# Optimization experiments

Measured on AMD Instinct MI355X. Metric: run time of the kernel, lower is better.

## Reference

```python
import jax, jax.numpy as jnp
import numpy as np

B, C, L, H, T, W = 512, 256, 256, 512, 16, 8  # batch, num_channels, seq_len, hidden_dim, timestep, windows


def setup_inputs() -> dict:
    key = jax.random.key(0)
    ks = jax.random.split(key, 8)
    s = 0.02
    return {
        "features_aug2": jax.random.normal(ks[0], (B, C, L), jnp.float32),
        "c_t": jax.random.normal(ks[1], (B, W, H), jnp.float32),
        "Wk_w": jax.random.normal(ks[2], (T, C, H), jnp.float32) * s,
        "Wk_b": jnp.zeros((T, C), jnp.float32),
        "pw1": jax.random.normal(ks[3], (C // 2, H), jnp.float32) * s,
        "pb1": jnp.zeros((C // 2,), jnp.float32),
        "bn_gamma": jnp.ones((C // 2,), jnp.float32),
        "bn_beta": jnp.zeros((C // 2,), jnp.float32),
        "pw2": jax.random.normal(ks[4], (C // 4, C // 2), jnp.float32) * s,
        "pb2": jnp.zeros((C // 4,), jnp.float32),
        "t_sample": 100,
    }


def reference(features_aug2, c_t, Wk_w, Wk_b, pw1, pb1, bn_gamma, bn_beta, pw2, pb2, t_sample):
    z2 = jnp.transpose(features_aug2, (0, 2, 1))            # [B, L, C]
    seq_len = z2.shape[1]
    Tn, Cn = Wk_w.shape[0], Wk_w.shape[1]
    Wn = c_t.shape[1]
    Bn = c_t.shape[0]

    # encode_samples: window slices of z_aug2 at offsets t+1 .. t+T (clipped to seq end)
    starts = jnp.minimum(t_sample + 1 + jnp.arange(Tn), seq_len - Wn)  # [T]
    idx = starts[:, None] + jnp.arange(Wn)                   # [T, W]
    encode = jnp.transpose(z2[:, idx, :], (1, 0, 2, 3))      # [T, B, W, C]

    # pred[i] = Wk[i](c_t): batched linear over all timesteps
    pred = jnp.einsum('bwh,tch->tbwc', c_t, Wk_w) + Wk_b[:, None, None, :]  # [T, B, W, C]

    # fused InfoNCE: all T*W pairwise (B x B) score matrices at once
    scores = jnp.einsum('tbwc,tawc->twba', encode, pred)     # [T, W, B, B]
    logp = jax.nn.log_softmax(scores, axis=-1)               # LogSoftmax over dim=1 of each [B,B] (torch implicit dim)
    diag = jnp.diagonal(logp, axis1=-2, axis2=-1)            # [T, W, B]
    nce = -jnp.sum(diag) / (Bn * Tn * Wn)

    # projection head on c_t.reshape(-1, H): Linear -> BatchNorm1d (train stats) -> ReLU -> Linear
    x = c_t.reshape(-1, c_t.shape[-1])                       # [B*W, H]
    h1 = x @ pw1.T + pb1                                     # [B*W, C/2]
    mean = jnp.mean(h1, axis=0)
    var = jnp.mean((h1 - mean) ** 2, axis=0)                 # biased variance (BN train mode)
    h1 = (h1 - mean) * jax.lax.rsqrt(var + 1e-5) * bn_gamma + bn_beta
    h1 = jax.nn.relu(h1)
    proj = h1 @ pw2.T + pb2                                  # [B*W, C/4]
    return nce, proj
```

## Files before the change

kernel.cpp:

```cpp
#include <hip/hip_runtime.h>

#define B_SZ 512
#define C_CH 256
#define L_SEQ 256
#define H_DIM 512
#define T_STEP 16
#define W_WIN 8
#define NSLAB 24
#define NCE_SHIFT 40.0f

typedef __attribute__((ext_vector_type(8))) short short8;
typedef __attribute__((ext_vector_type(4))) float f32x4;

#define GLOBAL_U32 const __attribute__((address_space(1))) unsigned int*
#define LDS_U32 __attribute__((address_space(3))) unsigned int*
#define ASYNC_COPY16(g, l) \
  __builtin_amdgcn_global_load_lds((GLOBAL_U32)(const void*)(g), (LDS_U32)(void*)(l), 16, 0, 0)

#define BARRIER __builtin_amdgcn_s_barrier()
#define SCHEDB  __builtin_amdgcn_sched_barrier(0)
#define LGK0 do { asm volatile("s_waitcnt lgkmcnt(0)" ::: "memory"); __builtin_amdgcn_sched_barrier(0); } while (0)

__device__ inline unsigned short f2bf(float x) {
  unsigned u = __float_as_uint(x);
  u = (u + 0x7FFFu + ((u >> 16) & 1u)) >> 16;
  return (unsigned short)u;
}

__global__ __launch_bounds__(256) void prep(const float* __restrict__ ct,
                                            const float* __restrict__ wk,
                                            const float* __restrict__ pw1,
                                            unsigned short* __restrict__ ctb,
                                            unsigned short* __restrict__ wkb,
                                            unsigned short* __restrict__ pw1b,
                                            float* __restrict__ bnp1,
                                            float* __restrict__ bnp2,
                                            float* __restrict__ out) {
  int b = blockIdx.x;
  if (b == 4160) {
    if (threadIdx.x < 128) { bnp1[threadIdx.x] = 0.f; bnp2[threadIdx.x] = 0.f; }
    if (threadIdx.x == 0) out[0] = 0.f;
    return;
  }
  const float* s;
  unsigned short* d;
  int base;
  if (b < 2048)      { s = ct;  d = ctb;  base = b * 1024; }
  else if (b < 4096) { s = wk;  d = wkb;  base = (b - 2048) * 1024; }
  else               { s = pw1; d = pw1b; base = (b - 4096) * 1024; }
  int i = base + threadIdx.x * 4;
  float4 v = ((const float4*)s)[i >> 2];
  ushort4 o;
  o.x = f2bf(v.x); o.y = f2bf(v.y); o.z = f2bf(v.z); o.w = f2bf(v.w);
  ((ushort4*)d)[i >> 2] = o;
}

__global__ __launch_bounds__(256) void build_slabs2(const float* __restrict__ f,
                                                    unsigned short* __restrict__ F,
                                                    const int* __restrict__ tsp) {
  const int ts = tsp[0];
  const int lmin = min(ts + 1, L_SEQ - W_WIN);
  const int b = blockIdx.x;
  const int c = threadIdx.x;
  const float* src = f + ((size_t)b * C_CH + c) * L_SEQ;
  float v[NSLAB];
#pragma unroll
  for (int lp = 0; lp < NSLAB; lp++) {
    int l = lmin + lp;
    v[lp] = (l < L_SEQ) ? src[l] : 0.f;
  }
#pragma unroll
  for (int lp = 0; lp < NSLAB; lp++)
    F[((size_t)lp * B_SZ + b) * C_CH + c] = f2bf(v[lp]);
}

#define PHASE(BUF, H, MH, STAGE_STMT) do {                                              \
    const int hb_ = ((BUF) * 2 + (H)) * 8192;                                           \
    short8 af_[4];                                                                      \
    _Pragma("unroll") for (int mq = 0; mq < 4; mq++)                                    \
      af_[mq] = *(const short8*)&Al[hb_ + abase + ((MH) * 4 + mq) * 512];               \
    if ((MH) == 0) {                                                                    \
      _Pragma("unroll") for (int n = 0; n < 4; n++)                                     \
        bf[n] = *(const short8*)&Bl[hb_ + bbase + n * 512];                             \
    }                                                                                   \
    STAGE_STMT;                                                                         \
    BARRIER;                                                                            \
    LGK0;                                                                               \
    __builtin_amdgcn_s_setprio(1);                                                      \
    _Pragma("unroll") for (int mq = 0; mq < 4; mq++)                                    \
    _Pragma("unroll") for (int n = 0; n < 4; n++)                                       \
      acc[(MH) * 4 + mq][n] =                                                           \
          __builtin_amdgcn_mfma_f32_16x16x32_bf16(af_[mq], bf[n], acc[(MH)*4+mq][n], 0, 0, 0); \
    __builtin_amdgcn_s_setprio(0);                                                      \
  } while (0)

template <int NT>
__device__ __forceinline__ void gemm256(unsigned short* Al, unsigned short* Bl,
                                        const unsigned short* __restrict__ A,
                                        const unsigned short* __restrict__ B,
                                        int Kst, f32x4 (&acc)[8][4]) {
  const int tid = threadIdx.x;
  const int wv = tid >> 6, lane = tid & 63, quad = lane >> 4, l15 = lane & 15;
  const int wm = wv >> 2, wn = wv & 3;
  const int qsw = (lane & 3) ^ ((lane >> 2) & 3);
  const int qs8 = (quad ^ (l15 & 3)) * 8;
  const int abase = (wm * 128 + l15) * 32 + qs8;
  const int bbase = (wn * 64 + l15) * 32 + qs8;

  auto stage = [&](int buf, int h, int kt) {
    const int kc = kt * 64 + h * 32 + qsw * 8;
#pragma unroll
    for (int i = 0; i < 2; i++) {
      int g = wv + i * 8;
      int row = g * 16 + (lane >> 2);
      ASYNC_COPY16(A + (size_t)row * Kst + kc, Al + ((buf * 2 + h) * 8192) + g * 512);
      ASYNC_COPY16(B + (size_t)row * Kst + kc, Bl + ((buf * 2 + h) * 8192) + g * 512);
    }
  };

  short8 bf[4];
  stage(0, 0, 0); stage(0, 1, 0); stage(1, 0, 1); stage(1, 1, 1);
  asm volatile("s_waitcnt vmcnt(8)" ::: "memory");
  BARRIER; SCHEDB;

  for (int k = 0; k < NT; k++) {
    const int cur = k & 1;
    PHASE(cur, 0, 0, { if (k >= 1 && k + 1 < NT) stage((k + 1) & 1, 1, k + 1); });
    BARRIER; SCHEDB;
    PHASE(cur, 0, 1, {});
    BARRIER; SCHEDB;
    PHASE(cur, 1, 0, { if (k + 2 < NT) stage(cur, 0, k + 2); });
    BARRIER; SCHEDB;
    PHASE(cur, 1, 1, {});
    if (k < NT - 2)       asm volatile("s_waitcnt vmcnt(4)" ::: "memory");
    else if (k == NT - 2) asm volatile("s_waitcnt vmcnt(0)" ::: "memory");
    BARRIER; SCHEDB;
  }
}

__global__ __launch_bounds__(512, 2) void pred_gemm(const unsigned short* __restrict__ A,
                                                    const unsigned short* __restrict__ Bt,
                                                    const float* __restrict__ bias,
                                                    unsigned short* __restrict__ pred) {
  __shared__ unsigned short Al[32768];
  __shared__ unsigned short Bl[32768];
  const int tid = threadIdx.x;
  const int wv = tid >> 6, lane = tid & 63, quad = lane >> 4, l15 = lane & 15;
  const int wm = wv >> 2, wn = wv & 3;
  const int M0 = (blockIdx.x >> 4) * 256, N0 = (blockIdx.x & 15) * 256;

  f32x4 acc[8][4];
#pragma unroll
  for (int m = 0; m < 8; m++)
#pragma unroll
    for (int n = 0; n < 4; n++) acc[m][n] = (f32x4){0.f, 0.f, 0.f, 0.f};

  gemm256<8>(Al, Bl, A + (size_t)M0 * 512, Bt + (size_t)N0 * 512, 512, acc);

  float bvs[4];
#pragma unroll
  for (int n = 0; n < 4; n++) bvs[n] = bias[N0 + wn * 64 + n * 16 + l15];
  unsigned short* cstash = wm ? Bl : Al;
#pragma unroll
  for (int m = 0; m < 8; m++)
#pragma unroll
    for (int n = 0; n < 4; n++) {
      int cc = wn * 64 + n * 16 + l15;
#pragma unroll
      for (int r = 0; r < 4; r++) {
        int rl = (m * 16 + quad * 4 + r);
        cstash[rl * 256 + cc] = f2bf(acc[m][n][r] + bvs[n]);
      }
    }
  BARRIER;
  const int tq = N0 >> 8, a0 = M0 >> 3;
  for (int idx = tid; idx < 256 * 32; idx += 512) {
    int rl = idx >> 5, seg = idx & 31;
    short8 v = *(const short8*)((rl < 128 ? Al : Bl) + (rl & 127) * 256 + seg * 8);
    int a = a0 + (rl >> 3), w_ = rl & 7;
    *(short8*)&pred[(((size_t)tq * 8 + w_) * 512 + a) * 256 + seg * 8] = v;
  }
}

__global__ __launch_bounds__(512, 2) void scores_gemm(const unsigned short* __restrict__ F,
                                                      const unsigned short* __restrict__ pred,
                                                      const int* __restrict__ tsp,
                                                      float* __restrict__ rowsum_p,
                                                      float* __restrict__ diagv) {
  __shared__ unsigned short Al[32768];
  __shared__ unsigned short Bl[32768];
  const int tid = threadIdx.x;
  const int wv = tid >> 6, lane = tid & 63, quad = lane >> 4, l15 = lane & 15;
  const int wm = wv >> 2, wn = wv & 3;
  const int swz = (blockIdx.x & 7) * 64 + (blockIdx.x >> 3);
  const int tw = swz >> 2, rb = (swz >> 1) & 1, cb = swz & 1;
  const int t = tw >> 3, w_ = tw & 7;
  const int ts = tsp[0];
  const int lmin = min(ts + 1, L_SEQ - W_WIN);
  const int lp = min(ts + 1 + t, L_SEQ - W_WIN) + w_ - lmin;
  const unsigned short* A = F + (size_t)lp * (B_SZ * C_CH) + (size_t)rb * 256 * C_CH;
  const unsigned short* Bt = pred + (size_t)tw * (B_SZ * C_CH) + (size_t)cb * 256 * C_CH;

  f32x4 acc[8][4];
#pragma unroll
  for (int m = 0; m < 8; m++)
#pragma unroll
    for (int n = 0; n < 4; n++) acc[m][n] = (f32x4){0.f, 0.f, 0.f, 0.f};

  gemm256<4>(Al, Bl, A, Bt, 256, acc);

#pragma unroll
  for (int m = 0; m < 8; m++) {
#pragma unroll
    for (int r = 0; r < 4; r++) {
      float e = 0.f;
#pragma unroll
      for (int n = 0; n < 4; n++) e += __expf(acc[m][n][r] - NCE_SHIFT);
      e += __shfl_xor(e, 1);
      e += __shfl_xor(e, 2);
      e += __shfl_xor(e, 4);
      e += __shfl_xor(e, 8);
      if (l15 == 0) {
        int b = rb * 256 + wm * 128 + m * 16 + quad * 4 + r;
        rowsum_p[((size_t)tw * 8 + cb * 4 + wn) * B_SZ + b] = e;
      }
    }
  }
  if (rb == cb) {
#pragma unroll
    for (int m = 0; m < 8; m++)
#pragma unroll
      for (int n = 0; n < 4; n++)
#pragma unroll
        for (int r = 0; r < 4; r++) {
          int d = wm * 128 + m * 16 + quad * 4 + r - wn * 64 - n * 16;
          if (d == l15) {
            int b = rb * 256 + wm * 128 + m * 16 + quad * 4 + r;
            diagv[(size_t)tw * B_SZ + b] = acc[m][n][r];
          }
        }
  }
}

__global__ __launch_bounds__(256) void gemm_h1(const unsigned short* __restrict__ A,
                                               const unsigned short* __restrict__ Bt,
                                               const float* __restrict__ bias,
                                               float* __restrict__ outf,
                                               float* __restrict__ bnp1,
                                               float* __restrict__ bnp2, int K) {
  __shared__ __align__(16) unsigned short As[128 * 64];
  __shared__ __align__(16) unsigned short Bs[128 * 64];
  const int tid = threadIdx.x;
  const int wv = tid >> 6, lane = tid & 63, quad = lane >> 4, l15 = lane & 15;
  const int wm = wv >> 1, wn = wv & 1;
  const int M0 = blockIdx.x * 128, N0 = 0;

  f32x4 acc[4][4];
#pragma unroll
  for (int i = 0; i < 4; i++)
#pragma unroll
    for (int j = 0; j < 4; j++) acc[i][j] = (f32x4){0.f, 0.f, 0.f, 0.f};

  for (int k0 = 0; k0 < K; k0 += 64) {
#pragma unroll
    for (int i = 0; i < 4; i++) {
      int chunk = (i * 4 + wv) * 64 + lane;
      int row = chunk >> 3, off = chunk & 7;
      ASYNC_COPY16(A + (size_t)(M0 + row) * K + k0 + off * 8, &As[(size_t)(i * 4 + wv) * 512]);
      ASYNC_COPY16(Bt + (size_t)(N0 + row) * K + k0 + off * 8, &Bs[(size_t)(i * 4 + wv) * 512]);
    }
    __syncthreads();
#pragma unroll
    for (int kk = 0; kk < 64; kk += 32) {
      short8 af[4], bfr[4];
#pragma unroll
      for (int i = 0; i < 4; i++)
        af[i] = *(const short8*)&As[(wm * 64 + i * 16 + l15) * 64 + kk + quad * 8];
#pragma unroll
      for (int j = 0; j < 4; j++)
        bfr[j] = *(const short8*)&Bs[(wn * 64 + j * 16 + l15) * 64 + kk + quad * 8];
#pragma unroll
      for (int i = 0; i < 4; i++)
#pragma unroll
        for (int j = 0; j < 4; j++)
          acc[i][j] = __builtin_amdgcn_mfma_f32_16x16x32_bf16(af[i], bfr[j], acc[i][j], 0, 0, 0);
    }
    __syncthreads();
  }

  float st1[4], st2[4];
#pragma unroll
  for (int j = 0; j < 4; j++) { st1[j] = 0.f; st2[j] = 0.f; }
#pragma unroll
  for (int i = 0; i < 4; i++) {
    int rbase = M0 + wm * 64 + i * 16 + quad * 4;
#pragma unroll
    for (int j = 0; j < 4; j++) {
      int cc = wn * 64 + j * 16 + l15;
      float bv = bias[cc];
#pragma unroll
      for (int r = 0; r < 4; r++) {
        int rr = rbase + r;
        float v = acc[i][j][r] + bv;
        outf[(size_t)rr * 128 + cc] = v;
        st1[j] += v;
        st2[j] += v * v;
      }
    }
  }
  __shared__ float red1[2][128], red2[2][128];
#pragma unroll
  for (int j = 0; j < 4; j++) {
    float a1 = st1[j], a2 = st2[j];
    a1 += __shfl_xor(a1, 16); a1 += __shfl_xor(a1, 32);
    a2 += __shfl_xor(a2, 16); a2 += __shfl_xor(a2, 32);
    if (quad == 0) {
      red1[wm][wn * 64 + j * 16 + l15] = a1;
      red2[wm][wn * 64 + j * 16 + l15] = a2;
    }
  }
  __syncthreads();
  if (tid < 128) {
    atomicAdd(&bnp1[tid], red1[0][tid] + red1[1][tid]);
    atomicAdd(&bnp2[tid], red2[0][tid] + red2[1][tid]);
  }
}

__global__ __launch_bounds__(256) void nce_rows(const float* __restrict__ rowsum_p,
                                                const float* __restrict__ diagv,
                                                float* __restrict__ out) {
  int gid = blockIdx.x * 256 + threadIdx.x;
  float s = 0.f;
  for (int i = gid; i < 65536; i += 16384) {
    int tw = i >> 9, b = i & 511;
    float rs = 0.f;
#pragma unroll
    for (int p = 0; p < 8; p++) rs += rowsum_p[((size_t)tw * 8 + p) * B_SZ + b];
    s += logf(rs) + NCE_SHIFT - diagv[i];
  }
#pragma unroll
  for (int off = 1; off < 64; off <<= 1) s += __shfl_xor(s, off);
  __shared__ float r[4];
  if ((threadIdx.x & 63) == 0) r[threadIdx.x >> 6] = s;
  __syncthreads();
  if (threadIdx.x == 0)
    atomicAdd(out, (r[0] + r[1] + r[2] + r[3]) * (1.f / 65536.f));
}

__global__ __launch_bounds__(256) void proj2(const float* __restrict__ h1,
                                             const float* __restrict__ bnp1,
                                             const float* __restrict__ bnp2,
                                             const float* __restrict__ g,
                                             const float* __restrict__ bta,
                                             const float* __restrict__ pw2,
                                             const float* __restrict__ pb2,
                                             float* __restrict__ out) {
  __shared__ float hsT[128][68];
  __shared__ float pw2T[128][68];
  __shared__ float scs[128], shs[128];
  const int tid = threadIdx.x;
  for (int idx = tid; idx < 64 * 128; idx += 256) {
    int oc = idx >> 7, k = idx & 127;
    pw2T[k][oc] = pw2[idx];
  }
  if (tid < 128) {
    float mean = bnp1[tid] * (1.f / 4096.f);
    float var = bnp2[tid] * (1.f / 4096.f) - mean * mean;
    float scale = g[tid] * rsqrtf(var + 1e-5f);
    scs[tid] = scale;
    shs[tid] = bta[tid] - mean * scale;
  }
  __syncthreads();
  const int r0 = blockIdx.x * 64;
  for (int idx = tid; idx < 64 * 128; idx += 256) {
    int r = idx >> 7, k = idx & 127;
    float v = h1[(size_t)(r0 + r) * 128 + k];
    hsT[k][r] = fmaxf(v * scs[k] + shs[k], 0.f);
  }
  __syncthreads();
  const int tx = tid & 15, ty = tid >> 4;
  float acc[4][4] = {};
  for (int k = 0; k < 128; k++) {
    f32x4 hv = *(const f32x4*)&hsT[k][ty * 4];
    f32x4 wv = *(const f32x4*)&pw2T[k][tx * 4];
#pragma unroll
    for (int i = 0; i < 4; i++)
#pragma unroll
      for (int j = 0; j < 4; j++) acc[i][j] += hv[i] * wv[j];
  }
#pragma unroll
  for (int i = 0; i < 4; i++) {
    int rr = r0 + ty * 4 + i;
#pragma unroll
    for (int j = 0; j < 4; j++)
      out[(size_t)rr * 64 + tx * 4 + j] = acc[i][j] + pb2[tx * 4 + j];
  }
}

extern "C" void kernel_launch(void* const* d_in, const int* in_sizes, int n_in,
                              void* d_out, int out_size, void* d_ws, size_t ws_size,
                              hipStream_t stream) {
  const float* features = (const float*)d_in[0];
  const float* c_t      = (const float*)d_in[1];
  const float* Wk_w     = (const float*)d_in[2];
  const float* Wk_b     = (const float*)d_in[3];
  const float* pw1      = (const float*)d_in[4];
  const float* pb1      = (const float*)d_in[5];
  const float* bn_gamma = (const float*)d_in[6];
  const float* bn_beta  = (const float*)d_in[7];
  const float* pw2      = (const float*)d_in[8];
  const float* pb2      = (const float*)d_in[9];
  const int*   tsp      = (const int*)d_in[10];
  float* out = (float*)d_out;

  char* ws = (char*)d_ws;
  size_t off = 0;
  auto carve = [&](size_t bytes) { void* p = ws + off; off += (bytes + 255) & ~(size_t)255; return p; };
  unsigned short* ct_bf  = (unsigned short*)carve((size_t)4096 * 512 * 2);
  unsigned short* wk_bf  = (unsigned short*)carve((size_t)4096 * 512 * 2);
  unsigned short* pw1_bf = (unsigned short*)carve((size_t)128 * 512 * 2);
  unsigned short* F      = (unsigned short*)carve((size_t)NSLAB * 512 * 256 * 2);
  unsigned short* pred   = (unsigned short*)carve((size_t)16 * 8 * 512 * 256 * 2);
  float* h1       = (float*)carve((size_t)4096 * 128 * 4);
  float* bnp1     = (float*)carve((size_t)128 * 4);
  float* bnp2     = (float*)carve((size_t)128 * 4);
  float* rowsum_p = (float*)carve((size_t)128 * 8 * 512 * 4);
  float* diagv    = (float*)carve((size_t)65536 * 4);

  prep<<<4161, 256, 0, stream>>>(c_t, Wk_w, pw1, ct_bf, wk_bf, pw1_bf, bnp1, bnp2, out);
  build_slabs2<<<512, 256, 0, stream>>>(features, F, tsp);

  pred_gemm<<<256, 512, 0, stream>>>(ct_bf, wk_bf, Wk_b, pred);
  gemm_h1<<<32, 256, 0, stream>>>(ct_bf, pw1_bf, pb1, h1, bnp1, bnp2, 512);

  scores_gemm<<<512, 512, 0, stream>>>(F, pred, tsp, rowsum_p, diagv);
  nce_rows<<<64, 256, 0, stream>>>(rowsum_p, diagv, out);

  proj2<<<64, 256, 0, stream>>>(h1, bnp1, bnp2, bn_gamma, bn_beta, pw2, pb2, out + 1);
}
```

Measured before the change: 287.3 us.

## Merge independent kernels into fewer launches and reuse A tile across column blocks

Folds the slab builder into the prep kernel, runs the h1 projection GEMM as extra blocks of the pred GEMM, and merges the NCE row reduction with the projection tail, cutting the pipeline from seven launches to four. scores_gemm now has each block loop over both column halves, halving the grid to 256 blocks and reusing the same F rows. Block index swizzles are added to pred GEMM for cache locality. The risk is less parallelism in scores_gemm and load imbalance from the small h1 blocks sharing the pred GEMM grid.

```diff
diff --git a/kernel.cpp b/kernel.cpp
--- a/kernel.cpp
+++ b/kernel.cpp
@@ -27,17 +27,37 @@
   return (unsigned short)u;
 }
 
-__global__ __launch_bounds__(256) void prep(const float* __restrict__ ct,
-                                            const float* __restrict__ wk,
-                                            const float* __restrict__ pw1,
-                                            unsigned short* __restrict__ ctb,
-                                            unsigned short* __restrict__ wkb,
-                                            unsigned short* __restrict__ pw1b,
-                                            float* __restrict__ bnp1,
-                                            float* __restrict__ bnp2,
-                                            float* __restrict__ out) {
-  int b = blockIdx.x;
-  if (b == 4160) {
+__global__ __launch_bounds__(256) void prep_all(const float* __restrict__ ct,
+                                                const float* __restrict__ wk,
+                                                const float* __restrict__ pw1,
+                                                const float* __restrict__ features,
+                                                const int* __restrict__ tsp,
+                                                unsigned short* __restrict__ ctb,
+                                                unsigned short* __restrict__ wkb,
+                                                unsigned short* __restrict__ pw1b,
+                                                unsigned short* __restrict__ F,
+                                                float* __restrict__ bnp1,
+                                                float* __restrict__ bnp2,
+                                                float* __restrict__ out) {
+  int blk = blockIdx.x;
+  if (blk >= 4161) {
+    const int ts = tsp[0];
+    const int lmin = min(ts + 1, L_SEQ - W_WIN);
+    const int b = blk - 4161;
+    const int c = threadIdx.x;
+    const float* src = features + ((size_t)b * C_CH + c) * L_SEQ;
+    float v[NSLAB];
+#pragma unroll
+    for (int lp = 0; lp < NSLAB; lp++) {
+      int l = lmin + lp;
+      v[lp] = (l < L_SEQ) ? src[l] : 0.f;
+    }
+#pragma unroll
+    for (int lp = 0; lp < NSLAB; lp++)
+      F[((size_t)lp * B_SZ + b) * C_CH + c] = f2bf(v[lp]);
+    return;
+  }
+  if (blk == 4160) {
     if (threadIdx.x < 128) { bnp1[threadIdx.x] = 0.f; bnp2[threadIdx.x] = 0.f; }
     if (threadIdx.x == 0) out[0] = 0.f;
     return;
@@ -45,33 +65,14 @@
   const float* s;
   unsigned short* d;
   int base;
-  if (b < 2048)      { s = ct;  d = ctb;  base = b * 1024; }
-  else if (b < 4096) { s = wk;  d = wkb;  base = (b - 2048) * 1024; }
-  else               { s = pw1; d = pw1b; base = (b - 4096) * 1024; }
+  if (blk < 2048)      { s = ct;  d = ctb;  base = blk * 1024; }
+  else if (blk < 4096) { s = wk;  d = wkb;  base = (blk - 2048) * 1024; }
+  else                 { s = pw1; d = pw1b; base = (blk - 4096) * 1024; }
   int i = base + threadIdx.x * 4;
   float4 v = ((const float4*)s)[i >> 2];
   ushort4 o;
   o.x = f2bf(v.x); o.y = f2bf(v.y); o.z = f2bf(v.z); o.w = f2bf(v.w);
   ((ushort4*)d)[i >> 2] = o;
-}
-
-__global__ __launch_bounds__(256) void build_slabs2(const float* __restrict__ f,
-                                                    unsigned short* __restrict__ F,
-                                                    const int* __restrict__ tsp) {
-  const int ts = tsp[0];
-  const int lmin = min(ts + 1, L_SEQ - W_WIN);
-  const int b = blockIdx.x;
-  const int c = threadIdx.x;
-  const float* src = f + ((size_t)b * C_CH + c) * L_SEQ;
-  float v[NSLAB];
-#pragma unroll
-  for (int lp = 0; lp < NSLAB; lp++) {
-    int l = lmin + lp;
-    v[lp] = (l < L_SEQ) ? src[l] : 0.f;
-  }
-#pragma unroll
-  for (int lp = 0; lp < NSLAB; lp++)
-    F[((size_t)lp * B_SZ + b) * C_CH + c] = f2bf(v[lp]);
 }
 
 #define PHASE(BUF, H, MH, STAGE_STMT) do {                                              \
@@ -138,16 +139,107 @@
   }
 }
 
-__global__ __launch_bounds__(512, 2) void pred_gemm(const unsigned short* __restrict__ A,
-                                                    const unsigned short* __restrict__ Bt,
-                                                    const float* __restrict__ bias,
-                                                    unsigned short* __restrict__ pred) {
+__global__ __launch_bounds__(512, 2) void mega_gemm(const unsigned short* __restrict__ ctb,
+                                                    const unsigned short* __restrict__ wkb,
+                                                    const float* __restrict__ wk_bias,
+                                                    const unsigned short* __restrict__ pw1b,
+                                                    const float* __restrict__ pb1,
+                                                    unsigned short* __restrict__ pred,
+                                                    float* __restrict__ h1,
+                                                    float* __restrict__ bnp1,
+                                                    float* __restrict__ bnp2) {
   __shared__ unsigned short Al[32768];
   __shared__ unsigned short Bl[32768];
   const int tid = threadIdx.x;
   const int wv = tid >> 6, lane = tid & 63, quad = lane >> 4, l15 = lane & 15;
+
+  if (blockIdx.x < 16) {
+    const int wm = wv >> 1, wn = wv & 1;
+    const int M0 = blockIdx.x * 256;
+    unsigned short* As = Al;
+    unsigned short* Bs = Bl;
+    f32x4 acc[4][4];
+#pragma unroll
+    for (int i = 0; i < 4; i++)
+#pragma unroll
+      for (int j = 0; j < 4; j++) acc[i][j] = (f32x4){0.f, 0.f, 0.f, 0.f};
+
+    for (int k0 = 0; k0 < 512; k0 += 64) {
+#pragma unroll
+      for (int i = 0; i < 4; i++) {
+        int chunk = i * 512 + tid;
+        int row = chunk >> 3, off = chunk & 7;
+        ASYNC_COPY16(ctb + (size_t)(M0 + row) * 512 + k0 + off * 8,
+                     &As[(size_t)(i * 512 + wv * 64) * 8]);
+      }
+#pragma unroll
+      for (int i = 0; i < 2; i++) {
+        int chunk = i * 512 + tid;
+        int row = chunk >> 3, off = chunk & 7;
+        ASYNC_COPY16(pw1b + (size_t)row * 512 + k0 + off * 8,
+                     &Bs[(size_t)(i * 512 + wv * 64) * 8]);
+      }
+      __syncthreads();
+#pragma unroll
+      for (int kk = 0; kk < 64; kk += 32) {
+        short8 af[4], bfr[4];
+#pragma unroll
+        for (int i = 0; i < 4; i++)
+          af[i] = *(const short8*)&As[(wm * 64 + i * 16 + l15) * 64 + kk + quad * 8];
+#pragma unroll
+        for (int j = 0; j < 4; j++)
+          bfr[j] = *(const short8*)&Bs[(wn * 64 + j * 16 + l15) * 64 + kk + quad * 8];
+#pragma unroll
+        for (int i = 0; i < 4; i++)
+#pragma unroll
+          for (int j = 0; j < 4; j++)
+            acc[i][j] = __builtin_amdgcn_mfma_f32_16x16x32_bf16(af[i], bfr[j], acc[i][j], 0, 0, 0);
+      }
+      __syncthreads();
+    }
+
+    float st1[4], st2[4];
+#pragma unroll
+    for (int j = 0; j < 4; j++) { st1[j] = 0.f; st2[j] = 0.f; }
+#pragma unroll
+    for (int i = 0; i < 4; i++) {
+      int rbase = M0 + wm * 64 + i * 16 + quad * 4;
+#pragma unroll
+      for (int j = 0; j < 4; j++) {
+        int cc = wn * 64 + j * 16 + l15;
+        float bv = pb1[cc];
+#pragma unroll
+        for (int r = 0; r < 4; r++) {
+          float v = acc[i][j][r] + bv;
+          h1[(size_t)(rbase + r) * 128 + cc] = v;
+          st1[j] += v;
+          st2[j] += v * v;
+        }
+      }
+    }
+    __shared__ float red1[4][128], red2[4][128];
+#pragma unroll
+    for (int j = 0; j < 4; j++) {
+      float a1 = st1[j], a2 = st2[j];
+      a1 += __shfl_xor(a1, 16); a1 += __shfl_xor(a1, 32);
+      a2 += __shfl_xor(a2, 16); a2 += __shfl_xor(a2, 32);
+      if (quad == 0) {
+        red1[wm][wn * 64 + j * 16 + l15] = a1;
+        red2[wm][wn * 64 + j * 16 + l15] = a2;
+      }
+    }
+    __syncthreads();
+    if (tid < 128) {
+      atomicAdd(&bnp1[tid], red1[0][tid] + red1[1][tid] + red1[2][tid] + red1[3][tid]);
+      atomicAdd(&bnp2[tid], red2[0][tid] + red2[1][tid] + red2[2][tid] + red2[3][tid]);
+    }
+    return;
+  }
+
   const int wm = wv >> 2, wn = wv & 3;
-  const int M0 = (blockIdx.x >> 4) * 256, N0 = (blockIdx.x & 15) * 256;
+  const int p = blockIdx.x - 16;
+  const int swz = (p & 7) * 32 + (p >> 3);
+  const int M0 = (swz >> 4) * 256, N0 = (swz & 15) * 256;
 
   f32x4 acc[8][4];
 #pragma unroll
@@ -155,11 +247,11 @@
 #pragma unroll
     for (int n = 0; n < 4; n++) acc[m][n] = (f32x4){0.f, 0.f, 0.f, 0.f};
 
-  gemm256<8>(Al, Bl, A + (size_t)M0 * 512, Bt + (size_t)N0 * 512, 512, acc);
+  gemm256<8>(Al, Bl, ctb + (size_t)M0 * 512, wkb + (size_t)N0 * 512, 512, acc);
 
   float bvs[4];
 #pragma unroll
-  for (int n = 0; n < 4; n++) bvs[n] = bias[N0 + wn * 64 + n * 16 + l15];
+  for (int n = 0; n < 4; n++) bvs[n] = wk_bias[N0 + wn * 64 + n * 16 + l15];
   unsigned short* cstash = wm ? Bl : Al;
 #pragma unroll
   for (int m = 0; m < 8; m++)
@@ -192,173 +284,93 @@
   const int tid = threadIdx.x;
   const int wv = tid >> 6, lane = tid & 63, quad = lane >> 4, l15 = lane & 15;
   const int wm = wv >> 2, wn = wv & 3;
-  const int swz = (blockIdx.x & 7) * 64 + (blockIdx.x >> 3);
-  const int tw = swz >> 2, rb = (swz >> 1) & 1, cb = swz & 1;
+  const int swz = (blockIdx.x & 7) * 32 + (blockIdx.x >> 3);
+  const int tw = swz >> 1, rb = swz & 1;
   const int t = tw >> 3, w_ = tw & 7;
   const int ts = tsp[0];
   const int lmin = min(ts + 1, L_SEQ - W_WIN);
   const int lp = min(ts + 1 + t, L_SEQ - W_WIN) + w_ - lmin;
   const unsigned short* A = F + (size_t)lp * (B_SZ * C_CH) + (size_t)rb * 256 * C_CH;
-  const unsigned short* Bt = pred + (size_t)tw * (B_SZ * C_CH) + (size_t)cb * 256 * C_CH;
-
-  f32x4 acc[8][4];
-#pragma unroll
-  for (int m = 0; m < 8; m++)
-#pragma unroll
-    for (int n = 0; n < 4; n++) acc[m][n] = (f32x4){0.f, 0.f, 0.f, 0.f};
-
-  gemm256<4>(Al, Bl, A, Bt, 256, acc);
-
-#pragma unroll
-  for (int m = 0; m < 8; m++) {
-#pragma unroll
-    for (int r = 0; r < 4; r++) {
-      float e = 0.f;
-#pragma unroll
-      for (int n = 0; n < 4; n++) e += __expf(acc[m][n][r] - NCE_SHIFT);
-      e += __shfl_xor(e, 1);
-      e += __shfl_xor(e, 2);
-      e += __shfl_xor(e, 4);
-      e += __shfl_xor(e, 8);
-      if (l15 == 0) {
-        int b = rb * 256 + wm * 128 + m * 16 + quad * 4 + r;
-        rowsum_p[((size_t)tw * 8 + cb * 4 + wn) * B_SZ + b] = e;
-      }
-    }
-  }
-  if (rb == cb) {
+
+  for (int cb = 0; cb < 2; cb++) {
+    const unsigned short* Bt = pred + (size_t)tw * (B_SZ * C_CH) + (size_t)cb * 256 * C_CH;
+    f32x4 acc[8][4];
 #pragma unroll
     for (int m = 0; m < 8; m++)
 #pragma unroll
-      for (int n = 0; n < 4; n++)
-#pragma unroll
-        for (int r = 0; r < 4; r++) {
-          int d = wm * 128 + m * 16 + quad * 4 + r - wn * 64 - n * 16;
-          if (d == l15) {
-            int b = rb * 256 + wm * 128 + m * 16 + quad * 4 + r;
-            diagv[(size_t)tw * B_SZ + b] = acc[m][n][r];
+      for (int n = 0; n < 4; n++) acc[m][n] = (f32x4){0.f, 0.f, 0.f, 0.f};
+
+    gemm256<4>(Al, Bl, A, Bt, 256, acc);
+
+#pragma unroll
+    for (int m = 0; m < 8; m++) {
+#pragma unroll
+      for (int r = 0; r < 4; r++) {
+        float e = 0.f;
+#pragma unroll
+        for (int n = 0; n < 4; n++) e += __expf(acc[m][n][r] - NCE_SHIFT);
+        e += __shfl_xor(e, 1);
+        e += __shfl_xor(e, 2);
+        e += __shfl_xor(e, 4);
+        e += __shfl_xor(e, 8);
+        if (l15 == 0) {
+          int b = rb * 256 + wm * 128 + m * 16 + quad * 4 + r;
+          rowsum_p[((size_t)tw * 8 + cb * 4 + wn) * B_SZ + b] = e;
+        }
+      }
+    }
+    if (rb == cb) {
+#pragma unroll
+      for (int m = 0; m < 8; m++)
+#pragma unroll
+        for (int n = 0; n < 4; n++)
+#pragma unroll
+          for (int r = 0; r < 4; r++) {
+            int d = wm * 128 + m * 16 + quad * 4 + r - wn * 64 - n * 16;
+            if (d == l15) {
+              int b = rb * 256 + wm * 128 + m * 16 + quad * 4 + r;
+              diagv[(size_t)tw * B_SZ + b] = acc[m][n][r];
+            }
           }
-        }
-  }
-}
-
-__global__ __launch_bounds__(256) void gemm_h1(const unsigned short* __restrict__ A,
-                                               const unsigned short* __restrict__ Bt,
-                                               const float* __restrict__ bias,
-                                               float* __restrict__ outf,
-                                               float* __restrict__ bnp1,
-                                               float* __restrict__ bnp2, int K) {
-  __shared__ __align__(16) unsigned short As[128 * 64];
-  __shared__ __align__(16) unsigned short Bs[128 * 64];
-  const int tid = threadIdx.x;
-  const int wv = tid >> 6, lane = tid & 63, quad = lane >> 4, l15 = lane & 15;
-  const int wm = wv >> 1, wn = wv & 1;
-  const int M0 = blockIdx.x * 128, N0 = 0;
-
-  f32x4 acc[4][4];
-#pragma unroll
-  for (int i = 0; i < 4; i++)
-#pragma unroll
-    for (int j = 0; j < 4; j++) acc[i][j] = (f32x4){0.f, 0.f, 0.f, 0.f};
-
-  for (int k0 = 0; k0 < K; k0 += 64) {
-#pragma unroll
-    for (int i = 0; i < 4; i++) {
-      int chunk = (i * 4 + wv) * 64 + lane;
-      int row = chunk >> 3, off = chunk & 7;
-      ASYNC_COPY16(A + (size_t)(M0 + row) * K + k0 + off * 8, &As[(size_t)(i * 4 + wv) * 512]);
-      ASYNC_COPY16(Bt + (size_t)(N0 + row) * K + k0 + off * 8, &Bs[(size_t)(i * 4 + wv) * 512]);
-    }
-    __syncthreads();
-#pragma unroll
-    for (int kk = 0; kk < 64; kk += 32) {
-      short8 af[4], bfr[4];
-#pragma unroll
-      for (int i = 0; i < 4; i++)
-        af[i] = *(const short8*)&As[(wm * 64 + i * 16 + l15) * 64 + kk + quad * 8];
-#pragma unroll
-      for (int j = 0; j < 4; j++)
-        bfr[j] = *(const short8*)&Bs[(wn * 64 + j * 16 + l15) * 64 + kk + quad * 8];
-#pragma unroll
-      for (int i = 0; i < 4; i++)
-#pragma unroll
-        for (int j = 0; j < 4; j++)
-          acc[i][j] = __builtin_amdgcn_mfma_f32_16x16x32_bf16(af[i], bfr[j], acc[i][j], 0, 0, 0);
-    }
-    __syncthreads();
-  }
-
-  float st1[4], st2[4];
-#pragma unroll
-  for (int j = 0; j < 4; j++) { st1[j] = 0.f; st2[j] = 0.f; }
-#pragma unroll
-  for (int i = 0; i < 4; i++) {
-    int rbase = M0 + wm * 64 + i * 16 + quad * 4;
-#pragma unroll
-    for (int j = 0; j < 4; j++) {
-      int cc = wn * 64 + j * 16 + l15;
-      float bv = bias[cc];
-#pragma unroll
-      for (int r = 0; r < 4; r++) {
-        int rr = rbase + r;
-        float v = acc[i][j][r] + bv;
-        outf[(size_t)rr * 128 + cc] = v;
-        st1[j] += v;
-        st2[j] += v * v;
-      }
-    }
-  }
-  __shared__ float red1[2][128], red2[2][128];
-#pragma unroll
-  for (int j = 0; j < 4; j++) {
-    float a1 = st1[j], a2 = st2[j];
-    a1 += __shfl_xor(a1, 16); a1 += __shfl_xor(a1, 32);
-    a2 += __shfl_xor(a2, 16); a2 += __shfl_xor(a2, 32);
-    if (quad == 0) {
-      red1[wm][wn * 64 + j * 16 + l15] = a1;
-      red2[wm][wn * 64 + j * 16 + l15] = a2;
-    }
-  }
-  __syncthreads();
-  if (tid < 128) {
-    atomicAdd(&bnp1[tid], red1[0][tid] + red1[1][tid]);
-    atomicAdd(&bnp2[tid], red2[0][tid] + red2[1][tid]);
-  }
-}
-
-__global__ __launch_bounds__(256) void nce_rows(const float* __restrict__ rowsum_p,
-                                                const float* __restrict__ diagv,
-                                                float* __restrict__ out) {
-  int gid = blockIdx.x * 256 + threadIdx.x;
-  float s = 0.f;
-  for (int i = gid; i < 65536; i += 16384) {
-    int tw = i >> 9, b = i & 511;
-    float rs = 0.f;
-#pragma unroll
-    for (int p = 0; p < 8; p++) rs += rowsum_p[((size_t)tw * 8 + p) * B_SZ + b];
-    s += logf(rs) + NCE_SHIFT - diagv[i];
-  }
-#pragma unroll
-  for (int off = 1; off < 64; off <<= 1) s += __shfl_xor(s, off);
-  __shared__ float r[4];
-  if ((threadIdx.x & 63) == 0) r[threadIdx.x >> 6] = s;
-  __syncthreads();
-  if (threadIdx.x == 0)
-    atomicAdd(out, (r[0] + r[1] + r[2] + r[3]) * (1.f / 65536.f));
-}
-
-__global__ __launch_bounds__(256) void proj2(const float* __restrict__ h1,
-                                             const float* __restrict__ bnp1,
-                                             const float* __restrict__ bnp2,
-                                             const float* __restrict__ g,
-                                             const float* __restrict__ bta,
-                                             const float* __restrict__ pw2,
-                                             const float* __restrict__ pb2,
-                                             float* __restrict__ out) {
+    }
+  }
+}
+
+__global__ __launch_bounds__(256) void tail(const float* __restrict__ rowsum_p,
+                                            const float* __restrict__ diagv,
+                                            const float* __restrict__ h1,
+                                            const float* __restrict__ bnp1,
+                                            const float* __restrict__ bnp2,
+                                            const float* __restrict__ g,
+                                            const float* __restrict__ bta,
+                                            const float* __restrict__ pw2,
+                                            const float* __restrict__ pb2,
+                                            float* __restrict__ out) {
   __shared__ float hsT[128][68];
   __shared__ float pw2T[128][68];
   __shared__ float scs[128], shs[128];
+  __shared__ float r4[4];
   const int tid = threadIdx.x;
+
+  if (blockIdx.x >= 64) {
+    int gid = (blockIdx.x - 64) * 256 + tid;
+    float s = 0.f;
+    for (int i = gid; i < 65536; i += 16384) {
+      int tw = i >> 9, b = i & 511;
+      float rs = 0.f;
+#pragma unroll
+      for (int p = 0; p < 8; p++) rs += rowsum_p[((size_t)tw * 8 + p) * B_SZ + b];
+      s += logf(rs) + NCE_SHIFT - diagv[i];
+    }
+#pragma unroll
+    for (int off = 1; off < 64; off <<= 1) s += __shfl_xor(s, off);
+    if ((tid & 63) == 0) r4[tid >> 6] = s;
+    __syncthreads();
+    if (tid == 0)
+      atomicAdd(out, (r4[0] + r4[1] + r4[2] + r4[3]) * (1.f / 65536.f));
+    return;
+  }
+
   for (int idx = tid; idx < 64 * 128; idx += 256) {
     int oc = idx >> 7, k = idx & 127;
     pw2T[k][oc] = pw2[idx];
@@ -382,18 +394,19 @@
   float acc[4][4] = {};
   for (int k = 0; k < 128; k++) {
     f32x4 hv = *(const f32x4*)&hsT[k][ty * 4];
-    f32x4 wv = *(const f32x4*)&pw2T[k][tx * 4];
+    f32x4 wvv = *(const f32x4*)&pw2T[k][tx * 4];
 #pragma unroll
     for (int i = 0; i < 4; i++)
 #pragma unroll
-      for (int j = 0; j < 4; j++) acc[i][j] += hv[i] * wv[j];
-  }
+      for (int j = 0; j < 4; j++) acc[i][j] += hv[i] * wvv[j];
+  }
+  float* proj_out = out + 1;
 #pragma unroll
   for (int i = 0; i < 4; i++) {
     int rr = r0 + ty * 4 + i;
 #pragma unroll
     for (int j = 0; j < 4; j++)
-      out[(size_t)rr * 64 + tx * 4 + j] = acc[i][j] + pb2[tx * 4 + j];
+      proj_out[(size_t)rr * 64 + tx * 4 + j] = acc[i][j] + pb2[tx * 4 + j];
   }
 }
 
@@ -427,14 +440,11 @@
   float* rowsum_p = (float*)carve((size_t)128 * 8 * 512 * 4);
   float* diagv    = (float*)carve((size_t)65536 * 4);
 
-  prep<<<4161, 256, 0, stream>>>(c_t, Wk_w, pw1, ct_bf, wk_bf, pw1_bf, bnp1, bnp2, out);
-  build_slabs2<<<512, 256, 0, stream>>>(features, F, tsp);
-
-  pred_gemm<<<256, 512, 0, stream>>>(ct_bf, wk_bf, Wk_b, pred);
-  gemm_h1<<<32, 256, 0, stream>>>(ct_bf, pw1_bf, pb1, h1, bnp1, bnp2, 512);
-
-  scores_gemm<<<512, 512, 0, stream>>>(F, pred, tsp, rowsum_p, diagv);
-  nce_rows<<<64, 256, 0, stream>>>(rowsum_p, diagv, out);
-
-  proj2<<<64, 256, 0, stream>>>(h1, bnp1, bnp2, bn_gamma, bn_beta, pw2, pb2, out + 1);
-}
+  prep_all<<<4673, 256, 0, stream>>>(c_t, Wk_w, pw1, features, tsp,
+                                     ct_bf, wk_bf, pw1_bf, F, bnp1, bnp2, out);
+  mega_gemm<<<272, 512, 0, stream>>>(ct_bf, wk_bf, Wk_b, pw1_bf, pb1,
+                                     pred, h1, bnp1, bnp2);
+  scores_gemm<<<256, 512, 0, stream>>>(F, pred, tsp, rowsum_p, diagv);
+  tail<<<128, 256, 0, stream>>>(rowsum_p, diagv, h1, bnp1, bnp2,
+                                bn_gamma, bn_beta, pw2, pb2, out);
+}
```

Measured after the change: 312.7 us. 8.8% more time.
